# Kernel optimization log

Hardware: AMD Instinct MI355X
Metric: run time of the kernel (lower is better)

## Reference

```python
import jax, jax.numpy as jnp
import numpy as np

GROUP_SIZE = 64
QMAX = 7.0   # int4 symmetric: clamp(round(x/s), -8, 7), zero-point = 0
QMIN = -8.0
EPS = 1e-8


def _group_quant_dequant(t, group_size):
    """Symmetric per-group int4 quantize + dequantize along the last dim.

    t: [..., F] with F % group_size == 0
    Returns dequantized tensor of same shape (equals q_int * scale, which is
    mathematically what the packed int4 GEMM with inline scale dequant computes).
    """
    shp = t.shape
    tg = t.reshape(shp[:-1] + (shp[-1] // group_size, group_size))
    scale = jnp.max(jnp.abs(tg), axis=-1, keepdims=True) / QMAX
    scale = jnp.maximum(scale, EPS)
    q = jnp.clip(jnp.round(tg / scale), QMIN, QMAX)
    return (q * scale).reshape(shp)


def setup_inputs() -> dict:
    key = jax.random.key(0)
    k1, k2 = jax.random.split(key)
    x = jax.random.normal(k1, (8192, 4096), dtype=jnp.float32)
    weight = jax.random.normal(k2, (4096, 4096), dtype=jnp.float32) * 0.02
    return {"x": x, "weight": weight}


def reference(x, weight):
    # ActQuantizerGS: per-token, per-group-of-64 symmetric int4 quant of x.
    x_dq = _group_quant_dequant(x, GROUP_SIZE)          # [T, K]
    # WeightQuantizer + LinearFLHGS: per-(out_channel, group) symmetric int4
    # weight quant; GEMM with inline scale dequant. Because scales are constant
    # within each group, int-accumulate-then-scale == dequant-then-matmul.
    w_dq = _group_quant_dequant(weight, GROUP_SIZE)     # [O, K]
    return x_dq @ w_dq.T                                # [T, O]
```

## Files before the change

### kernel.cpp

```cpp
#include <hip/hip_runtime.h>
#include <hip/hip_bf16.h>
#include <stdint.h>


typedef __bf16 bf16x8 __attribute__((ext_vector_type(8)));
typedef float f32x4 __attribute__((ext_vector_type(4)));

static __device__ __forceinline__ uint16_t f32_to_bf16_rne(float f) {
    uint32_t u = __float_as_uint(f);
    uint32_t r = (u + 0x7fffu + ((u >> 16) & 1u)) >> 16;
    return (uint16_t)r;
}

__global__ void quant_kernel(const float* __restrict__ in,
                             uint16_t* __restrict__ out, int total4) {
    int nthreads = gridDim.x * blockDim.x;
    int t = blockIdx.x * blockDim.x + threadIdx.x;
    for (int i = t; i < total4; i += nthreads) {
        float4 v = ((const float4*)in)[i];
        float amax = fmaxf(fmaxf(fabsf(v.x), fabsf(v.y)),
                           fmaxf(fabsf(v.z), fabsf(v.w)));
        #pragma unroll
        for (int m = 1; m <= 8; m <<= 1)
            amax = fmaxf(amax, __shfl_xor(amax, m, 64));
        float s = fmaxf(amax * (1.0f / 7.0f), 1e-8f);
        float q0 = fminf(fmaxf(rintf(v.x / s), -8.0f), 7.0f);
        float q1 = fminf(fmaxf(rintf(v.y / s), -8.0f), 7.0f);
        float q2 = fminf(fmaxf(rintf(v.z / s), -8.0f), 7.0f);
        float q3 = fminf(fmaxf(rintf(v.w / s), -8.0f), 7.0f);
        ushort4 o;
        o.x = f32_to_bf16_rne(q0 * s);
        o.y = f32_to_bf16_rne(q1 * s);
        o.z = f32_to_bf16_rne(q2 * s);
        o.w = f32_to_bf16_rne(q3 * s);
        ((ushort4*)out)[i] = o;
    }
}

#define BM 128
#define BN 128
#define BK 64

__global__ __launch_bounds__(256, 2) void gemm_kernel(
        const uint16_t* __restrict__ A, const uint16_t* __restrict__ B,
        float* __restrict__ C, int M, int N, int K) {
    __shared__ uint16_t As[BM * BK];
    __shared__ uint16_t Bs[BN * BK];

    int nwg = gridDim.x;
    int bid = blockIdx.x;
    int swz = bid;
    if ((nwg & 7) == 0) {
        int cpx = nwg >> 3;
        swz = (bid & 7) * cpx + (bid >> 3);
    }
    int nbn = N / BN;
    int bm = swz / nbn, bn = swz % nbn;

    int tid = threadIdx.x;
    int lane = tid & 63;
    int wid = tid >> 6;
    int wr = wid >> 1, wc = wid & 1;

    f32x4 acc[4][4] = {};

    const int rowA0 = bm * BM;
    const int colB0 = bn * BN;

    int srow = lane >> 3;
    int scol = ((lane & 7) ^ (lane >> 3)) << 3;

    for (int kt = 0; kt < K; kt += BK) {
        #pragma unroll
        for (int j = 0; j < 4; ++j) {
            int rblk = (wid * 4 + j) * 8;
            const uint16_t* ga =
                A + (size_t)(rowA0 + rblk + srow) * K + kt + scol;
            const uint16_t* gb =
                B + (size_t)(colB0 + rblk + srow) * K + kt + scol;
            uint16_t* la = As + rblk * BK;
            uint16_t* lb = Bs + rblk * BK;
            __builtin_amdgcn_global_load_lds(
                (const __attribute__((address_space(1))) void*)ga,
                (__attribute__((address_space(3))) void*)la, 16, 0, 0);
            __builtin_amdgcn_global_load_lds(
                (const __attribute__((address_space(1))) void*)gb,
                (__attribute__((address_space(3))) void*)lb, 16, 0, 0);
        }
        __syncthreads();

        #pragma unroll
        for (int ks = 0; ks < 2; ++ks) {
            bf16x8 af[4], bfr[4];
            int rl = lane & 15;
            int c = ks * 4 + (lane >> 4);
            #pragma unroll
            for (int mi = 0; mi < 4; ++mi) {
                int row = wr * 64 + mi * 16 + rl;
                af[mi] = *(const bf16x8*)(As + row * BK + ((c ^ (row & 7)) << 3));
            }
            #pragma unroll
            for (int ni = 0; ni < 4; ++ni) {
                int row = wc * 64 + ni * 16 + rl;
                bfr[ni] = *(const bf16x8*)(Bs + row * BK + ((c ^ (row & 7)) << 3));
            }
            #pragma unroll
            for (int mi = 0; mi < 4; ++mi)
                #pragma unroll
                for (int ni = 0; ni < 4; ++ni)
                    acc[mi][ni] = __builtin_amdgcn_mfma_f32_16x16x32_bf16(
                        af[mi], bfr[ni], acc[mi][ni], 0, 0, 0);
        }
        __syncthreads();
    }

    int cl = lane & 15;
    int rq = (lane >> 4) * 4;
    #pragma unroll
    for (int mi = 0; mi < 4; ++mi) {
        #pragma unroll
        for (int ni = 0; ni < 4; ++ni) {
            int row = rowA0 + wr * 64 + mi * 16 + rq;
            int col = colB0 + wc * 64 + ni * 16 + cl;
            float* cp = C + (size_t)row * N + col;
            #pragma unroll
            for (int r = 0; r < 4; ++r)
                cp[(size_t)r * N] = acc[mi][ni][r];
        }
    }
}

extern "C" void kernel_launch(void* const* d_in, const int* in_sizes, int n_in,
                              void* d_out, int out_size, void* d_ws, size_t ws_size,
                              hipStream_t stream) {
    const float* x = (const float*)d_in[0];
    const float* w = (const float*)d_in[1];
    float* out = (float*)d_out;

    const int K = 4096;
    const int T = in_sizes[0] / K;
    const int O = in_sizes[1] / K;

    uint16_t* xq = (uint16_t*)d_ws;
    uint16_t* wq = (uint16_t*)((char*)d_ws + (size_t)T * K * 2);

    quant_kernel<<<2048, 256, 0, stream>>>(x, xq, (T * K) >> 2);
    quant_kernel<<<2048, 256, 0, stream>>>(w, wq, (O * K) >> 2);

    int nwg = (T / BM) * (O / BN);
    gemm_kernel<<<nwg, 256, 0, stream>>>(xq, wq, out, T, O, K);
}
```

Measured before the change: 344.0 us.

## Use 256x256 tiles with 8 waves and double-buffered LDS pipeline

After: 306.2 us. -11.0%, faster.

```diff
diff --git a/kernel.cpp b/kernel.cpp
--- a/kernel.cpp
+++ b/kernel.cpp
@@ -37,15 +37,17 @@
     }
 }
 
-#define BM 128
-#define BN 128
+#define BM 256
+#define BN 256
 #define BK 64
 
-__global__ __launch_bounds__(256, 2) void gemm_kernel(
+__global__ __launch_bounds__(512, 2) void gemm8_kernel(
         const uint16_t* __restrict__ A, const uint16_t* __restrict__ B,
         float* __restrict__ C, int M, int N, int K) {
-    __shared__ uint16_t As[BM * BK];
-    __shared__ uint16_t Bs[BN * BK];
+    __shared__ uint16_t As[2][2][128 * 64];
+    __shared__ uint16_t Bs[2][2][128 * 64];
+
+    const int NTt = K >> 6;
 
     int nwg = gridDim.x;
     int bid = blockIdx.x;
@@ -60,9 +62,8 @@
     int tid = threadIdx.x;
     int lane = tid & 63;
     int wid = tid >> 6;
-    int wr = wid >> 1, wc = wid & 1;
-
-    f32x4 acc[4][4] = {};
+    int wm = wid >> 2;
+    int wn = wid & 3;
 
     const int rowA0 = bm * BM;
     const int colB0 = bn * BN;
@@ -70,64 +71,164 @@
     int srow = lane >> 3;
     int scol = ((lane & 7) ^ (lane >> 3)) << 3;
 
-    for (int kt = 0; kt < K; kt += BK) {
-        #pragma unroll
-        for (int j = 0; j < 4; ++j) {
-            int rblk = (wid * 4 + j) * 8;
-            const uint16_t* ga =
-                A + (size_t)(rowA0 + rblk + srow) * K + kt + scol;
-            const uint16_t* gb =
-                B + (size_t)(colB0 + rblk + srow) * K + kt + scol;
-            uint16_t* la = As + rblk * BK;
-            uint16_t* lb = Bs + rblk * BK;
+    int rl = lane & 15;
+    int cg = lane >> 4;
+    int coff[2];
+    coff[0] = ((0 + cg) ^ (rl & 7)) << 3;
+    coff[1] = ((4 + cg) ^ (rl & 7)) << 3;
+
+    f32x4 acc[8][4] = {};
+
+    auto stageA = [&](int buf, int half, int t) {
+        #pragma unroll
+        for (int j = 0; j < 2; ++j) {
+            int rowin = wid * 16 + j * 8;
+            const uint16_t* g = A + (size_t)(rowA0 + half * 128 + rowin + srow) * K
+                                  + t * 64 + scol;
+            uint16_t* l = &As[buf][half][rowin * 64];
             __builtin_amdgcn_global_load_lds(
-                (const __attribute__((address_space(1))) void*)ga,
-                (__attribute__((address_space(3))) void*)la, 16, 0, 0);
+                (const __attribute__((address_space(1))) void*)g,
+                (__attribute__((address_space(3))) void*)l, 16, 0, 0);
+        }
+    };
+    auto stageB = [&](int buf, int half, int t) {
+        #pragma unroll
+        for (int j = 0; j < 2; ++j) {
+            int rowin = wid * 16 + j * 8;
+            const uint16_t* g = B + (size_t)(colB0 + half * 128 + rowin + srow) * K
+                                  + t * 64 + scol;
+            uint16_t* l = &Bs[buf][half][rowin * 64];
             __builtin_amdgcn_global_load_lds(
-                (const __attribute__((address_space(1))) void*)gb,
-                (__attribute__((address_space(3))) void*)lb, 16, 0, 0);
+                (const __attribute__((address_space(1))) void*)g,
+                (__attribute__((address_space(3))) void*)l, 16, 0, 0);
         }
-        __syncthreads();
-
-        #pragma unroll
-        for (int ks = 0; ks < 2; ++ks) {
-            bf16x8 af[4], bfr[4];
-            int rl = lane & 15;
-            int c = ks * 4 + (lane >> 4);
-            #pragma unroll
-            for (int mi = 0; mi < 4; ++mi) {
-                int row = wr * 64 + mi * 16 + rl;
-                af[mi] = *(const bf16x8*)(As + row * BK + ((c ^ (row & 7)) << 3));
-            }
-            #pragma unroll
-            for (int ni = 0; ni < 4; ++ni) {
-                int row = wc * 64 + ni * 16 + rl;
-                bfr[ni] = *(const bf16x8*)(Bs + row * BK + ((c ^ (row & 7)) << 3));
-            }
-            #pragma unroll
-            for (int mi = 0; mi < 4; ++mi)
-                #pragma unroll
-                for (int ni = 0; ni < 4; ++ni)
+    };
+
+    stageA(0, 0, 0); stageA(0, 1, 0);
+    stageB(0, 0, 0); stageB(0, 1, 0);
+    if (NTt > 1) {
+        stageB(1, 0, 1); stageB(1, 1, 1);
+        asm volatile("s_waitcnt vmcnt(4)" ::: "memory");
+    } else {
+        asm volatile("s_waitcnt vmcnt(0)" ::: "memory");
+    }
+    asm volatile("" ::: "memory");
+    __builtin_amdgcn_s_barrier();
+    asm volatile("" ::: "memory");
+
+    bf16x8 aLo[4][2], aHi[4][2], bLo[2][2], bHi[2][2];
+    const int bhalf = wn >> 1;
+    const int brow0 = (wn & 1) * 64;
+
+#define PHASE_MID() \
+    asm volatile("" ::: "memory"); \
+    __builtin_amdgcn_s_barrier(); \
+    asm volatile("s_waitcnt lgkmcnt(0)" ::: "memory"); \
+    __builtin_amdgcn_sched_barrier(0); \
+    __builtin_amdgcn_s_setprio(1);
+
+#define PHASE_END() \
+    __builtin_amdgcn_s_setprio(0); \
+    asm volatile("" ::: "memory"); \
+    __builtin_amdgcn_s_barrier(); \
+    asm volatile("" ::: "memory");
+
+    for (int t = 0; t < NTt; ++t) {
+        int cb = t & 1, nb = cb ^ 1;
+
+        #pragma unroll
+        for (int mi = 0; mi < 4; ++mi)
+            #pragma unroll
+            for (int ks = 0; ks < 2; ++ks)
+                aLo[mi][ks] = *(const bf16x8*)&As[cb][wm][(mi * 16 + rl) * 64 + coff[ks]];
+        #pragma unroll
+        for (int ni = 0; ni < 2; ++ni)
+            #pragma unroll
+            for (int ks = 0; ks < 2; ++ks)
+                bLo[ni][ks] = *(const bf16x8*)&Bs[cb][bhalf][(brow0 + ni * 16 + rl) * 64 + coff[ks]];
+        if (t + 1 < NTt) stageA(nb, 0, t + 1);
+        PHASE_MID();
+        #pragma unroll
+        for (int mi = 0; mi < 4; ++mi)
+            #pragma unroll
+            for (int ni = 0; ni < 2; ++ni)
+                #pragma unroll
+                for (int ks = 0; ks < 2; ++ks)
                     acc[mi][ni] = __builtin_amdgcn_mfma_f32_16x16x32_bf16(
-                        af[mi], bfr[ni], acc[mi][ni], 0, 0, 0);
-        }
-        __syncthreads();
+                        aLo[mi][ks], bLo[ni][ks], acc[mi][ni], 0, 0, 0);
+        PHASE_END();
+
+        #pragma unroll
+        for (int ni = 0; ni < 2; ++ni)
+            #pragma unroll
+            for (int ks = 0; ks < 2; ++ks)
+                bHi[ni][ks] = *(const bf16x8*)&Bs[cb][bhalf][(brow0 + (ni + 2) * 16 + rl) * 64 + coff[ks]];
+        if (t + 1 < NTt) stageA(nb, 1, t + 1);
+        PHASE_MID();
+        #pragma unroll
+        for (int mi = 0; mi < 4; ++mi)
+            #pragma unroll
+            for (int ni = 0; ni < 2; ++ni)
+                #pragma unroll
+                for (int ks = 0; ks < 2; ++ks)
+                    acc[mi][ni + 2] = __builtin_amdgcn_mfma_f32_16x16x32_bf16(
+                        aLo[mi][ks], bHi[ni][ks], acc[mi][ni + 2], 0, 0, 0);
+        PHASE_END();
+
+        #pragma unroll
+        for (int mi = 0; mi < 4; ++mi)
+            #pragma unroll
+            for (int ks = 0; ks < 2; ++ks)
+                aHi[mi][ks] = *(const bf16x8*)&As[cb][wm][((mi + 4) * 16 + rl) * 64 + coff[ks]];
+        if (t + 2 < NTt) stageB(cb, 0, t + 2);
+        PHASE_MID();
+        #pragma unroll
+        for (int mi = 0; mi < 4; ++mi)
+            #pragma unroll
+            for (int ni = 0; ni < 2; ++ni)
+                #pragma unroll
+                for (int ks = 0; ks < 2; ++ks)
+                    acc[mi + 4][ni] = __builtin_amdgcn_mfma_f32_16x16x32_bf16(
+                        aHi[mi][ks], bLo[ni][ks], acc[mi + 4][ni], 0, 0, 0);
+        PHASE_END();
+
+        if (t + 2 < NTt) stageB(cb, 1, t + 2);
+        asm volatile("" ::: "memory");
+        __builtin_amdgcn_s_barrier();
+        __builtin_amdgcn_sched_barrier(0);
+        __builtin_amdgcn_s_setprio(1);
+        #pragma unroll
+        for (int mi = 0; mi < 4; ++mi)
+            #pragma unroll
+            for (int ni = 0; ni < 2; ++ni)
+                #pragma unroll
+                for (int ks = 0; ks < 2; ++ks)
+                    acc[mi + 4][ni + 2] = __builtin_amdgcn_mfma_f32_16x16x32_bf16(
+                        aHi[mi][ks], bHi[ni][ks], acc[mi + 4][ni + 2], 0, 0, 0);
+        __builtin_amdgcn_s_setprio(0);
+        if (t + 2 < NTt) asm volatile("s_waitcnt vmcnt(4)" ::: "memory");
+        else             asm volatile("s_waitcnt vmcnt(0)" ::: "memory");
+        asm volatile("" ::: "memory");
+        __builtin_amdgcn_s_barrier();
+        asm volatile("" ::: "memory");
     }
 
     int cl = lane & 15;
     int rq = (lane >> 4) * 4;
     #pragma unroll
-    for (int mi = 0; mi < 4; ++mi) {
+    for (int mi = 0; mi < 8; ++mi) {
         #pragma unroll
         for (int ni = 0; ni < 4; ++ni) {
-            int row = rowA0 + wr * 64 + mi * 16 + rq;
-            int col = colB0 + wc * 64 + ni * 16 + cl;
+            int row = rowA0 + wm * 128 + mi * 16 + rq;
+            int col = colB0 + wn * 64 + ni * 16 + cl;
             float* cp = C + (size_t)row * N + col;
             #pragma unroll
             for (int r = 0; r < 4; ++r)
                 cp[(size_t)r * N] = acc[mi][ni][r];
         }
     }
+#undef PHASE_MID
+#undef PHASE_END
 }
 
 extern "C" void kernel_launch(void* const* d_in, const int* in_sizes, int n_in,
@@ -148,5 +249,5 @@
     quant_kernel<<<2048, 256, 0, stream>>>(w, wq, (O * K) >> 2);
 
     int nwg = (T / BM) * (O / BN);
-    gemm_kernel<<<nwg, 256, 0, stream>>>(xq, wq, out, T, O, K);
-}
+    gemm8_kernel<<<nwg, 512, 0, stream>>>(xq, wq, out, T, O, K);
+}
```

## Switch GEMM to int8 MFMA with per-group scale dequant and double-buffered LDS

Applied to the files above, without the earlier changes.

After: 791.2 us. +130.0%, slower.

```diff
diff --git a/kernel.cpp b/kernel.cpp
--- a/kernel.cpp
+++ b/kernel.cpp
@@ -3,49 +3,49 @@
 #include <stdint.h>
 
 
-typedef __bf16 bf16x8 __attribute__((ext_vector_type(8)));
-typedef float f32x4 __attribute__((ext_vector_type(4)));
-
-static __device__ __forceinline__ uint16_t f32_to_bf16_rne(float f) {
-    uint32_t u = __float_as_uint(f);
-    uint32_t r = (u + 0x7fffu + ((u >> 16) & 1u)) >> 16;
-    return (uint16_t)r;
-}
+typedef int   int32x4 __attribute__((ext_vector_type(4)));
+typedef float f32x4   __attribute__((ext_vector_type(4)));
 
 __global__ void quant_kernel(const float* __restrict__ in,
-                             uint16_t* __restrict__ out, int total4) {
-    int nthreads = gridDim.x * blockDim.x;
-    int t = blockIdx.x * blockDim.x + threadIdx.x;
-    for (int i = t; i < total4; i += nthreads) {
+                             int8_t* __restrict__ qout,
+                             float* __restrict__ sT,
+                             int total4, int nrows) {
+    int nth = gridDim.x * blockDim.x;
+    int t0 = blockIdx.x * blockDim.x + threadIdx.x;
+    for (int i = t0; i < total4; i += nth) {
         float4 v = ((const float4*)in)[i];
         float amax = fmaxf(fmaxf(fabsf(v.x), fabsf(v.y)),
                            fmaxf(fabsf(v.z), fabsf(v.w)));
         #pragma unroll
         for (int m = 1; m <= 8; m <<= 1)
             amax = fmaxf(amax, __shfl_xor(amax, m, 64));
-        float s = fmaxf(amax * (1.0f / 7.0f), 1e-8f);
-        float q0 = fminf(fmaxf(rintf(v.x / s), -8.0f), 7.0f);
-        float q1 = fminf(fmaxf(rintf(v.y / s), -8.0f), 7.0f);
-        float q2 = fminf(fmaxf(rintf(v.z / s), -8.0f), 7.0f);
-        float q3 = fminf(fmaxf(rintf(v.w / s), -8.0f), 7.0f);
-        ushort4 o;
-        o.x = f32_to_bf16_rne(q0 * s);
-        o.y = f32_to_bf16_rne(q1 * s);
-        o.z = f32_to_bf16_rne(q2 * s);
-        o.w = f32_to_bf16_rne(q3 * s);
-        ((ushort4*)out)[i] = o;
+        float s = fmaxf(amax / 7.0f, 1e-8f);
+        int q0 = (int)fminf(fmaxf(rintf(v.x / s), -8.0f), 7.0f);
+        int q1 = (int)fminf(fmaxf(rintf(v.y / s), -8.0f), 7.0f);
+        int q2 = (int)fminf(fmaxf(rintf(v.z / s), -8.0f), 7.0f);
+        int q3 = (int)fminf(fmaxf(rintf(v.w / s), -8.0f), 7.0f);
+        uint32_t packed = (uint32_t)(q0 & 255) | ((uint32_t)(q1 & 255) << 8) |
+                          ((uint32_t)(q2 & 255) << 16) | ((uint32_t)(q3 & 255) << 24);
+        ((uint32_t*)qout)[i] = packed;
+        if ((i & 15) == 0) {
+            int row = i >> 10;
+            int gir = (i & 1023) >> 4;
+            sT[(size_t)gir * nrows + row] = s;
+        }
     }
 }
 
-#define BM 128
-#define BN 128
-#define BK 64
-
-__global__ __launch_bounds__(256, 2) void gemm_kernel(
-        const uint16_t* __restrict__ A, const uint16_t* __restrict__ B,
+#define BM 256
+#define BN 256
+
+__global__ __launch_bounds__(512, 2) void gemm_kernel(
+        const int8_t* __restrict__ A, const int8_t* __restrict__ B,
+        const float* __restrict__ sAT, const float* __restrict__ sBT,
         float* __restrict__ C, int M, int N, int K) {
-    __shared__ uint16_t As[BM * BK];
-    __shared__ uint16_t Bs[BN * BK];
+    __shared__ int8_t As[2][256 * 64];
+    __shared__ int8_t Bs[2][256 * 64];
+
+    const int NTt = K >> 6;
 
     int nwg = gridDim.x;
     int bid = blockIdx.x;
@@ -60,68 +60,115 @@
     int tid = threadIdx.x;
     int lane = tid & 63;
     int wid = tid >> 6;
-    int wr = wid >> 1, wc = wid & 1;
-
-    f32x4 acc[4][4] = {};
+    int wm = wid >> 2;
+    int wn = wid & 3;
 
     const int rowA0 = bm * BM;
     const int colB0 = bn * BN;
 
-    int srow = lane >> 3;
-    int scol = ((lane & 7) ^ (lane >> 3)) << 3;
-
-    for (int kt = 0; kt < K; kt += BK) {
-        #pragma unroll
-        for (int j = 0; j < 4; ++j) {
-            int rblk = (wid * 4 + j) * 8;
-            const uint16_t* ga =
-                A + (size_t)(rowA0 + rblk + srow) * K + kt + scol;
-            const uint16_t* gb =
-                B + (size_t)(colB0 + rblk + srow) * K + kt + scol;
-            uint16_t* la = As + rblk * BK;
-            uint16_t* lb = Bs + rblk * BK;
+    int rl = lane & 15;
+    int cR = lane >> 4;
+    int rsw = ((cR ^ ((rl >> 1) & 3)) << 4);
+    int rq = cR * 4;
+
+    int sgc = (((lane & 3) ^ ((lane >> 3) & 3)) << 4);
+
+    f32x4 acc[8][4] = {};
+
+    const int8_t* Ag = A + (size_t)rowA0 * K;
+    const int8_t* Bg = B + (size_t)colB0 * K;
+
+    auto stage = [&](const int8_t* g0, int8_t* l0, int t) {
+        #pragma unroll
+        for (int j = 0; j < 2; ++j) {
+            int R0 = wid * 32 + j * 16;
+            const int8_t* g = g0 + (size_t)(R0 + (lane >> 2)) * K + t * 64 + sgc;
+            int8_t* l = l0 + R0 * 64;
             __builtin_amdgcn_global_load_lds(
-                (const __attribute__((address_space(1))) void*)ga,
-                (__attribute__((address_space(3))) void*)la, 16, 0, 0);
-            __builtin_amdgcn_global_load_lds(
-                (const __attribute__((address_space(1))) void*)gb,
-                (__attribute__((address_space(3))) void*)lb, 16, 0, 0);
-        }
-        __syncthreads();
-
-        #pragma unroll
-        for (int ks = 0; ks < 2; ++ks) {
-            bf16x8 af[4], bfr[4];
-            int rl = lane & 15;
-            int c = ks * 4 + (lane >> 4);
-            #pragma unroll
-            for (int mi = 0; mi < 4; ++mi) {
-                int row = wr * 64 + mi * 16 + rl;
-                af[mi] = *(const bf16x8*)(As + row * BK + ((c ^ (row & 7)) << 3));
-            }
+                (const __attribute__((address_space(1))) void*)g,
+                (__attribute__((address_space(3))) void*)l, 16, 0, 0);
+        }
+    };
+
+    stage(Ag, As[0], 0); stage(Bg, Bs[0], 0);
+    stage(Ag, As[1], 1); stage(Bg, Bs[1], 1);
+    asm volatile("s_waitcnt vmcnt(4)" ::: "memory");
+    asm volatile("" ::: "memory");
+    __builtin_amdgcn_s_barrier();
+    asm volatile("" ::: "memory");
+
+    const int32x4 zero = {0, 0, 0, 0};
+
+    for (int t = 0; t < NTt; ++t) {
+        int cb = t & 1;
+
+        int32x4 bv[4], av0[4], av1[4];
+        #pragma unroll
+        for (int ni = 0; ni < 4; ++ni)
+            bv[ni] = *(const int32x4*)&Bs[cb][(wn * 64 + ni * 16 + rl) * 64 + rsw];
+        #pragma unroll
+        for (int mi = 0; mi < 4; ++mi)
+            av0[mi] = *(const int32x4*)&As[cb][(wm * 128 + mi * 16 + rl) * 64 + rsw];
+        #pragma unroll
+        for (int mi = 0; mi < 4; ++mi)
+            av1[mi] = *(const int32x4*)&As[cb][(wm * 128 + 64 + mi * 16 + rl) * 64 + rsw];
+
+        float sbv[4];
+        #pragma unroll
+        for (int ni = 0; ni < 4; ++ni)
+            sbv[ni] = sBT[(size_t)t * N + colB0 + wn * 64 + ni * 16 + rl];
+        f32x4 sa0[4];
+        #pragma unroll
+        for (int mi = 0; mi < 4; ++mi)
+            sa0[mi] = *(const f32x4*)&sAT[(size_t)t * M + rowA0 + wm * 128 + mi * 16 + rq];
+
+        #pragma unroll
+        for (int mi = 0; mi < 4; ++mi) {
             #pragma unroll
             for (int ni = 0; ni < 4; ++ni) {
-                int row = wc * 64 + ni * 16 + rl;
-                bfr[ni] = *(const bf16x8*)(Bs + row * BK + ((c ^ (row & 7)) << 3));
+                int32x4 iv = __builtin_amdgcn_mfma_i32_16x16x64_i8(
+                    av0[mi], bv[ni], zero, 0, 0, 0);
+                #pragma unroll
+                for (int r = 0; r < 4; ++r)
+                    acc[mi][ni][r] += (float)iv[r] * sa0[mi][r] * sbv[ni];
             }
+        }
+
+        f32x4 sa1[4];
+        #pragma unroll
+        for (int mi = 0; mi < 4; ++mi)
+            sa1[mi] = *(const f32x4*)&sAT[(size_t)t * M + rowA0 + wm * 128 + 64 + mi * 16 + rq];
+
+        asm volatile("s_waitcnt lgkmcnt(0)" ::: "memory");
+        asm volatile("" ::: "memory");
+        __builtin_amdgcn_s_barrier();
+        asm volatile("" ::: "memory");
+        if (t + 2 < NTt) { stage(Ag, As[cb], t + 2); stage(Bg, Bs[cb], t + 2); }
+
+        #pragma unroll
+        for (int mi = 0; mi < 4; ++mi) {
             #pragma unroll
-            for (int mi = 0; mi < 4; ++mi)
+            for (int ni = 0; ni < 4; ++ni) {
+                int32x4 iv = __builtin_amdgcn_mfma_i32_16x16x64_i8(
+                    av1[mi], bv[ni], zero, 0, 0, 0);
                 #pragma unroll
-                for (int ni = 0; ni < 4; ++ni)
-                    acc[mi][ni] = __builtin_amdgcn_mfma_f32_16x16x32_bf16(
-                        af[mi], bfr[ni], acc[mi][ni], 0, 0, 0);
-        }
-        __syncthreads();
+                for (int r = 0; r < 4; ++r)
+                    acc[4 + mi][ni][r] += (float)iv[r] * sa1[mi][r] * sbv[ni];
+            }
+        }
+
+        asm volatile("" ::: "memory");
+        __builtin_amdgcn_s_barrier();
+        asm volatile("" ::: "memory");
     }
 
     int cl = lane & 15;
-    int rq = (lane >> 4) * 4;
     #pragma unroll
-    for (int mi = 0; mi < 4; ++mi) {
+    for (int mi = 0; mi < 8; ++mi) {
         #pragma unroll
         for (int ni = 0; ni < 4; ++ni) {
-            int row = rowA0 + wr * 64 + mi * 16 + rq;
-            int col = colB0 + wc * 64 + ni * 16 + cl;
+            int row = rowA0 + wm * 128 + mi * 16 + rq;
+            int col = colB0 + wn * 64 + ni * 16 + cl;
             float* cp = C + (size_t)row * N + col;
             #pragma unroll
             for (int r = 0; r < 4; ++r)
@@ -141,12 +188,14 @@
     const int T = in_sizes[0] / K;
     const int O = in_sizes[1] / K;
 
-    uint16_t* xq = (uint16_t*)d_ws;
-    uint16_t* wq = (uint16_t*)((char*)d_ws + (size_t)T * K * 2);
-
-    quant_kernel<<<2048, 256, 0, stream>>>(x, xq, (T * K) >> 2);
-    quant_kernel<<<2048, 256, 0, stream>>>(w, wq, (O * K) >> 2);
+    int8_t* qx  = (int8_t*)d_ws;
+    int8_t* qw  = qx + (size_t)T * K;
+    float*  sxT = (float*)(qw + (size_t)O * K);
+    float*  swT = sxT + (size_t)(K / 64) * T;
+
+    quant_kernel<<<2048, 256, 0, stream>>>(x, qx, sxT, (T * K) >> 2, T);
+    quant_kernel<<<2048, 256, 0, stream>>>(w, qw, swT, (O * K) >> 2, O);
 
     int nwg = (T / BM) * (O / BN);
-    gemm_kernel<<<nwg, 256, 0, stream>>>(xq, wq, out, T, O, K);
+    gemm_kernel<<<nwg, 512, 0, stream>>>(qx, qw, sxT, swT, out, T, O, K);
 }
```
